# Kernel optimization log

Hardware: AMD Instinct MI355X
Metric: run time of the kernel (lower is better)

## Reference

```python
import jax, jax.numpy as jnp
import numpy as np

P = 512       # protein_dim
D = 512       # drug_dim
N = 2000      # neighbors per layer
E = 300000    # binding edges per layer
ND = 100000   # total drugs
BASELINE = 6.0
LN_EPS = 1e-5


def setup_inputs() -> dict:
    key = jax.random.key(0)
    ks = jax.random.split(key, 24)
    inp = {
        "target_features": jax.random.normal(ks[0], (P,), jnp.float32),
        "form_features": jax.random.normal(ks[1], (N, P), jnp.float32),
        "role_features": jax.random.normal(ks[2], (N, P), jnp.float32),
        "form_neighbors": jnp.arange(N, dtype=jnp.int64) if jax.config.jax_enable_x64 else jnp.arange(N, dtype=jnp.int32),
        "role_neighbors": jnp.arange(N, dtype=jnp.int32),
        "form_binds_ei": jax.random.randint(ks[3], (2, E), 0, N, jnp.int32),
        "form_binds_y": jax.random.uniform(ks[4], (E,), jnp.float32) * 8.0 + 2.0,
        "role_binds_ei": jax.random.randint(ks[5], (2, E), 0, N, jnp.int32),
        "role_binds_y": jax.random.uniform(ks[6], (E,), jnp.float32) * 8.0 + 2.0,
        "drug_features": jax.random.normal(ks[7], (ND, D), jnp.float32),
    }
    inp["form_neighbors"] = jnp.arange(N, dtype=jnp.int32)
    attn_in = P * 2 + 16
    s1 = 1.0 / np.sqrt(attn_in)
    s2 = 1.0 / np.sqrt(64)
    sd = 1.0 / np.sqrt(D)
    sp = 1.0 / np.sqrt(P)
    inp["layer_emb"] = jax.random.normal(ks[8], (2, 16), jnp.float32)
    inp["W1"] = jax.random.uniform(ks[9], (attn_in, 64), jnp.float32, -s1, s1)
    inp["b1"] = jax.random.uniform(ks[10], (64,), jnp.float32, -s1, s1)
    inp["W2"] = jax.random.uniform(ks[11], (64, 1), jnp.float32, -s2, s2)
    inp["b2"] = jax.random.uniform(ks[12], (1,), jnp.float32, -s2, s2)
    inp["Wi1"] = jax.random.uniform(ks[13], (D, P), jnp.float32, -sd, sd)
    inp["bi1"] = jax.random.uniform(ks[14], (P,), jnp.float32, -sd, sd)
    inp["prelu_alpha"] = jnp.array(0.25, jnp.float32)
    inp["Wi2"] = jax.random.uniform(ks[15], (P, P), jnp.float32, -sp, sp)
    inp["bi2"] = jax.random.uniform(ks[16], (P,), jnp.float32, -sp, sp)
    inp["ln_gamma"] = jnp.ones((P,), jnp.float32)
    inp["ln_beta"] = jnp.zeros((P,), jnp.float32)
    return inp


def _pref_vectors(neighbor_ids, ei, y, drug_features):
    # Vectorized form of the per-neighbor masked gather-sum:
    # for each edge, find its neighbor slot (neighbor_ids is sorted);
    # edges whose src id is not a neighbor get zero weight.
    n = neighbor_ids.shape[0]
    pos = jnp.clip(jnp.searchsorted(neighbor_ids, ei[0]), 0, n - 1)
    valid = neighbor_ids[pos] == ei[0]
    w = jnp.where(valid, y - BASELINE, 0.0)              # [E]
    contrib = drug_features[ei[1]] * w[:, None]          # [E, D] gather (memory-bound)
    return jax.ops.segment_sum(contrib, pos, num_segments=n)  # [N, D]


def _attention(z_target, z_neighbors, l_vec, W1, b1, W2, b2):
    n = z_neighbors.shape[0]
    inp = jnp.concatenate(
        [jnp.broadcast_to(z_target, (n, z_target.shape[0])),
         z_neighbors,
         jnp.broadcast_to(l_vec, (n, l_vec.shape[0]))], axis=-1)  # [N, 2P+16]
    h = inp @ W1 + b1
    h = jnp.where(h > 0, h, 0.2 * h)  # LeakyReLU(0.2)
    return h @ W2 + b2                # [N, 1]


def reference(target_features, form_features, role_features, form_neighbors,
              role_neighbors, form_binds_ei, form_binds_y, role_binds_ei,
              role_binds_y, drug_features, layer_emb, W1, b1, W2, b2,
              Wi1, bi1, prelu_alpha, Wi2, bi2, ln_gamma, ln_beta):
    form_msgs = _pref_vectors(form_neighbors, form_binds_ei, form_binds_y, drug_features)
    role_msgs = _pref_vectors(role_neighbors, role_binds_ei, role_binds_y, drug_features)

    form_attn = _attention(target_features, form_features, layer_emb[0], W1, b1, W2, b2)
    role_attn = _attention(target_features, role_features, layer_emb[1], W1, b1, W2, b2)

    all_msgs = jnp.concatenate([form_msgs, role_msgs], axis=0)   # [2N, D]
    all_attn = jnp.concatenate([form_attn, role_attn], axis=0)   # [2N, 1]
    attn_weights = jax.nn.softmax(all_attn, axis=0)
    v_prior = jnp.sum(attn_weights * all_msgs, axis=0)           # [D]

    h = v_prior @ Wi1 + bi1
    h = jnp.where(h > 0, h, prelu_alpha * h)  # PReLU
    v = h @ Wi2 + bi2                          # [P]

    x = target_features + v
    mu = jnp.mean(x)
    var = jnp.mean(jnp.square(x - mu))
    z_refined = (x - mu) / jnp.sqrt(var + LN_EPS) * ln_gamma + ln_beta
    return (z_refined, form_msgs, role_msgs)
```

## Files before the change

### kernel.cpp

```cpp
#include <hip/hip_runtime.h>
#include <math.h>

static constexpr int PD = 512;
static constexpr float BASEV = 6.0f;
static constexpr int CAP = 320;

typedef float f4v __attribute__((ext_vector_type(4)));
typedef int   i4v __attribute__((ext_vector_type(4)));
typedef int   i2v __attribute__((ext_vector_type(2)));

__global__ __launch_bounds__(256) void front_kernel(
    const int* __restrict__ ei_f, const float* __restrict__ y_f,
    const int* __restrict__ ei_r, const float* __restrict__ y_r,
    const int* __restrict__ nb_f, const int* __restrict__ nb_r,
    const float* __restrict__ target, const float* __restrict__ formF,
    const float* __restrict__ roleF, const float* __restrict__ lemb,
    const float* __restrict__ W1, const float* __restrict__ b1,
    const float* __restrict__ W2, const float* __restrict__ b2,
    int N, int E, int AB, int EBf,
    int* __restrict__ cnt, int2* __restrict__ bins,
    float* __restrict__ logits) {
    __shared__ float sred[384];
    int b = blockIdx.x;
    if (b >= AB) {
        int b2 = b - AB;
        bool role = b2 >= EBf;
        const int* nb = role ? nb_r : nb_f;
        const int* ei = role ? ei_r : ei_f;
        const float* yy = role ? y_r : y_f;
        int base = (role ? b2 - EBf : b2) * 1024;
        int nb0 = nb[0];
#pragma unroll
        for (int r = 0; r < 4; r++) {
            int e = base + threadIdx.x + r * 256;
            if (e >= E) continue;
            int v = ei[e];
            int g = v - nb0; g = g < 0 ? 0 : (g >= N ? N - 1 : g);
            int pos;
            if (nb[g] == v && (g == 0 || nb[g - 1] < v)) {
                pos = g;
            } else {
                int lo = 0, hi = N;
                while (lo < hi) { int mid = (lo + hi) >> 1; if (nb[mid] < v) lo = mid + 1; else hi = mid; }
                pos = lo < N ? lo : N - 1;
                if (nb[pos] != v) continue;
            }
            int s = role ? N + pos : pos;
            float w = yy[e] - BASEV;
            int slot = atomicAdd(&cnt[s], 1);
            if (slot < CAP) {
                i2v val; val.x = ei[E + e]; val.y = __float_as_int(w);
                __builtin_nontemporal_store(val, reinterpret_cast<i2v*>(bins + (size_t)s * CAP + slot));
            }
        }
    } else {
        float* spart = sred;
        float* sc0 = spart + 256;
        float* sc1 = spart + 320;
        int jj = threadIdx.x & 63, ck = threadIdx.x >> 6;
        const float* Wc = W1 + jj;
        float tp = 0.f;
        int p0 = ck * 128;
        for (int p = p0; p < p0 + 128; p += 4) {
            float4 tv = *(const float4*)(target + p);
            tp += tv.x * Wc[(size_t)(p + 0) * 64] + tv.y * Wc[(size_t)(p + 1) * 64]
                + tv.z * Wc[(size_t)(p + 2) * 64] + tv.w * Wc[(size_t)(p + 3) * 64];
        }
        spart[ck * 64 + jj] = tp;
        __syncthreads();
        if (ck == 0) {
            float c = b1[jj] + spart[jj] + spart[64 + jj] + spart[128 + jj] + spart[192 + jj];
            float c0 = c, c1 = c;
            for (int q = 0; q < 16; q++) {
                float wq = Wc[(size_t)(2 * PD + q) * 64];
                c0 += lemb[q] * wq;
                c1 += lemb[16 + q] * wq;
            }
            sc0[jj] = c0; sc1[jj] = c1;
        }
        __syncthreads();
        int wave = threadIdx.x >> 6, lane = threadIdx.x & 63;
        int rr = b * 4 + wave;
        int nseg = 2 * N;
        if (rr >= nseg) return;
        bool rl = rr >= N;
        const float* z = rl ? roleF + (size_t)(rr - N) * PD : formF + (size_t)rr * PD;
        const float* Wz = W1 + (size_t)PD * 64 + lane;
        float hA = rl ? sc1[lane] : sc0[lane];
        float hB = 0.f, hC = 0.f, hD = 0.f;
        for (int p = 0; p < PD; p += 8) {
            float4 z0 = *(const float4*)(z + p);
            float4 z1 = *(const float4*)(z + p + 4);
            hA += z0.x * Wz[(size_t)(p + 0) * 64] + z0.y * Wz[(size_t)(p + 1) * 64];
            hB += z0.z * Wz[(size_t)(p + 2) * 64] + z0.w * Wz[(size_t)(p + 3) * 64];
            hC += z1.x * Wz[(size_t)(p + 4) * 64] + z1.y * Wz[(size_t)(p + 5) * 64];
            hD += z1.z * Wz[(size_t)(p + 6) * 64] + z1.w * Wz[(size_t)(p + 7) * 64];
        }
        float hh = (hA + hB) + (hC + hD);
        hh = hh > 0.f ? hh : 0.2f * hh;
        float vv = hh * W2[lane];
#pragma unroll
        for (int off = 32; off > 0; off >>= 1) vv += __shfl_down(vv, off, 64);
        if (lane == 0) logits[rr] = vv + b2[0];
    }
}

__global__ __launch_bounds__(128) void accum_kernel(const int* __restrict__ cnt,
                                                    const int2* __restrict__ bins,
                                                    const float* __restrict__ drug,
                                                    const float* __restrict__ logits,
                                                    int nseg,
                                                    float* __restrict__ sm,
                                                    float* __restrict__ msgs) {
    int b = blockIdx.x;
    int t = threadIdx.x;
    if (b == nseg) {
        __shared__ float red[128];
        float m = -1e30f;
        for (int s = t; s < nseg; s += 128) m = fmaxf(m, logits[s]);
        red[t] = m; __syncthreads();
        for (int o = 64; o > 0; o >>= 1) { if (t < o) red[t] = fmaxf(red[t], red[t + o]); __syncthreads(); }
        m = red[0]; __syncthreads();
        float sum = 0.f;
        for (int s = t; s < nseg; s += 128) sum += expf(logits[s] - m);
        red[t] = sum; __syncthreads();
        for (int o = 64; o > 0; o >>= 1) { if (t < o) red[t] += red[t + o]; __syncthreads(); }
        if (t == 0) { sm[0] = m; sm[1] = red[0]; }
        return;
    }
    int n = cnt[b]; n = n < CAP ? n : CAP;
    const int2* bb = bins + (size_t)b * CAP;
    float4 acc = make_float4(0.f, 0.f, 0.f, 0.f);
    int k = 0;
    for (; k + 15 < n; k += 16) {
        i4v q0 = __builtin_nontemporal_load(reinterpret_cast<const i4v*>(bb + k + 0));
        i4v q1 = __builtin_nontemporal_load(reinterpret_cast<const i4v*>(bb + k + 2));
        i4v q2 = __builtin_nontemporal_load(reinterpret_cast<const i4v*>(bb + k + 4));
        i4v q3 = __builtin_nontemporal_load(reinterpret_cast<const i4v*>(bb + k + 6));
        i4v q4 = __builtin_nontemporal_load(reinterpret_cast<const i4v*>(bb + k + 8));
        i4v q5 = __builtin_nontemporal_load(reinterpret_cast<const i4v*>(bb + k + 10));
        i4v q6 = __builtin_nontemporal_load(reinterpret_cast<const i4v*>(bb + k + 12));
        i4v q7 = __builtin_nontemporal_load(reinterpret_cast<const i4v*>(bb + k + 14));
        float4 d0 = ((const float4*)(drug + (size_t)q0.x * PD))[t];
        float4 d1 = ((const float4*)(drug + (size_t)q0.z * PD))[t];
        float4 d2 = ((const float4*)(drug + (size_t)q1.x * PD))[t];
        float4 d3 = ((const float4*)(drug + (size_t)q1.z * PD))[t];
        float4 d4 = ((const float4*)(drug + (size_t)q2.x * PD))[t];
        float4 d5 = ((const float4*)(drug + (size_t)q2.z * PD))[t];
        float4 d6 = ((const float4*)(drug + (size_t)q3.x * PD))[t];
        float4 d7 = ((const float4*)(drug + (size_t)q3.z * PD))[t];
        float4 d8 = ((const float4*)(drug + (size_t)q4.x * PD))[t];
        float4 d9 = ((const float4*)(drug + (size_t)q4.z * PD))[t];
        float4 da = ((const float4*)(drug + (size_t)q5.x * PD))[t];
        float4 db = ((const float4*)(drug + (size_t)q5.z * PD))[t];
        float4 dc = ((const float4*)(drug + (size_t)q6.x * PD))[t];
        float4 dd = ((const float4*)(drug + (size_t)q6.z * PD))[t];
        float4 de = ((const float4*)(drug + (size_t)q7.x * PD))[t];
        float4 df = ((const float4*)(drug + (size_t)q7.z * PD))[t];
        float w0 = __int_as_float(q0.y), w1 = __int_as_float(q0.w);
        float w2 = __int_as_float(q1.y), w3 = __int_as_float(q1.w);
        float w4 = __int_as_float(q2.y), w5 = __int_as_float(q2.w);
        float w6 = __int_as_float(q3.y), w7 = __int_as_float(q3.w);
        float w8 = __int_as_float(q4.y), w9 = __int_as_float(q4.w);
        float wa = __int_as_float(q5.y), wb = __int_as_float(q5.w);
        float wc = __int_as_float(q6.y), wd = __int_as_float(q6.w);
        float we = __int_as_float(q7.y), wf = __int_as_float(q7.w);
        acc.x += w0 * d0.x; acc.y += w0 * d0.y; acc.z += w0 * d0.z; acc.w += w0 * d0.w;
        acc.x += w1 * d1.x; acc.y += w1 * d1.y; acc.z += w1 * d1.z; acc.w += w1 * d1.w;
        acc.x += w2 * d2.x; acc.y += w2 * d2.y; acc.z += w2 * d2.z; acc.w += w2 * d2.w;
        acc.x += w3 * d3.x; acc.y += w3 * d3.y; acc.z += w3 * d3.z; acc.w += w3 * d3.w;
        acc.x += w4 * d4.x; acc.y += w4 * d4.y; acc.z += w4 * d4.z; acc.w += w4 * d4.w;
        acc.x += w5 * d5.x; acc.y += w5 * d5.y; acc.z += w5 * d5.z; acc.w += w5 * d5.w;
        acc.x += w6 * d6.x; acc.y += w6 * d6.y; acc.z += w6 * d6.z; acc.w += w6 * d6.w;
        acc.x += w7 * d7.x; acc.y += w7 * d7.y; acc.z += w7 * d7.z; acc.w += w7 * d7.w;
        acc.x += w8 * d8.x; acc.y += w8 * d8.y; acc.z += w8 * d8.z; acc.w += w8 * d8.w;
        acc.x += w9 * d9.x; acc.y += w9 * d9.y; acc.z += w9 * d9.z; acc.w += w9 * d9.w;
        acc.x += wa * da.x; acc.y += wa * da.y; acc.z += wa * da.z; acc.w += wa * da.w;
        acc.x += wb * db.x; acc.y += wb * db.y; acc.z += wb * db.z; acc.w += wb * db.w;
        acc.x += wc * dc.x; acc.y += wc * dc.y; acc.z += wc * dc.z; acc.w += wc * dc.w;
        acc.x += wd * dd.x; acc.y += wd * dd.y; acc.z += wd * dd.z; acc.w += wd * dd.w;
        acc.x += we * de.x; acc.y += we * de.y; acc.z += we * de.z; acc.w += we * de.w;
        acc.x += wf * df.x; acc.y += wf * df.y; acc.z += wf * df.z; acc.w += wf * df.w;
    }
    for (; k + 3 < n; k += 4) {
        i4v q0 = __builtin_nontemporal_load(reinterpret_cast<const i4v*>(bb + k + 0));
        i4v q1 = __builtin_nontemporal_load(reinterpret_cast<const i4v*>(bb + k + 2));
        float4 d0 = ((const float4*)(drug + (size_t)q0.x * PD))[t];
        float4 d1 = ((const float4*)(drug + (size_t)q0.z * PD))[t];
        float4 d2 = ((const float4*)(drug + (size_t)q1.x * PD))[t];
        float4 d3 = ((const float4*)(drug + (size_t)q1.z * PD))[t];
        float w0 = __int_as_float(q0.y), w1 = __int_as_float(q0.w);
        float w2 = __int_as_float(q1.y), w3 = __int_as_float(q1.w);
        acc.x += w0 * d0.x; acc.y += w0 * d0.y; acc.z += w0 * d0.z; acc.w += w0 * d0.w;
        acc.x += w1 * d1.x; acc.y += w1 * d1.y; acc.z += w1 * d1.z; acc.w += w1 * d1.w;
        acc.x += w2 * d2.x; acc.y += w2 * d2.y; acc.z += w2 * d2.z; acc.w += w2 * d2.w;
        acc.x += w3 * d3.x; acc.y += w3 * d3.y; acc.z += w3 * d3.z; acc.w += w3 * d3.w;
    }
    for (; k < n; k++) {
        int2 e0 = bb[k];
        float w0 = __int_as_float(e0.y);
        float4 d0 = ((const float4*)(drug + (size_t)e0.x * PD))[t];
        acc.x += w0 * d0.x; acc.y += w0 * d0.y; acc.z += w0 * d0.z; acc.w += w0 * d0.w;
    }
    f4v av; av.x = acc.x; av.y = acc.y; av.z = acc.z; av.w = acc.w;
    __builtin_nontemporal_store(av, reinterpret_cast<f4v*>(msgs + (size_t)b * PD) + t);
}

__global__ __launch_bounds__(128) void vprior_kernel(const float* __restrict__ logits,
                                                     const float* __restrict__ msgs,
                                                     const float* __restrict__ sm,
                                                     int nseg, float* __restrict__ v_prior) {
    int t = threadIdx.x;
    float m = sm[0];
    float inv = 1.f / sm[1];
    float4 acc = make_float4(0.f, 0.f, 0.f, 0.f);
    for (int s = blockIdx.x; s < nseg; s += gridDim.x) {
        float w = expf(logits[s] - m) * inv;
        float4 d = ((const float4*)(msgs + (size_t)s * PD))[t];
        acc.x += w * d.x; acc.y += w * d.y; acc.z += w * d.z; acc.w += w * d.w;
    }
    atomicAdd(&v_prior[4 * t + 0], acc.x);
    atomicAdd(&v_prior[4 * t + 1], acc.y);
    atomicAdd(&v_prior[4 * t + 2], acc.z);
    atomicAdd(&v_prior[4 * t + 3], acc.w);
}

__global__ __launch_bounds__(256) void mv1_kernel(const float* __restrict__ v_prior,
                                                  const float* __restrict__ Wi1,
                                                  float* __restrict__ h) {
    int b = blockIdx.x;
    int t = threadIdx.x;
    float2 acc = make_float2(0.f, 0.f);
    int d0 = b * 16;
    for (int d = d0; d < d0 + 16; d++) {
        float vd = v_prior[d];
        float2 w = ((const float2*)(Wi1 + (size_t)d * PD))[t];
        acc.x += vd * w.x; acc.y += vd * w.y;
    }
    atomicAdd(&h[2 * t + 0], acc.x);
    atomicAdd(&h[2 * t + 1], acc.y);
}

__global__ __launch_bounds__(256) void mv2_kernel(const float* __restrict__ h,
                                                  const float* __restrict__ bi1,
                                                  const float* __restrict__ alpha_p,
                                                  const float* __restrict__ Wi2,
                                                  float* __restrict__ v) {
    int b = blockIdx.x;
    int t = threadIdx.x;
    float alpha = alpha_p[0];
    float2 acc = make_float2(0.f, 0.f);
    int q0 = b * 16;
    for (int q = q0; q < q0 + 16; q++) {
        float hq = h[q] + bi1[q];
        hq = hq > 0.f ? hq : alpha * hq;
        float2 w = ((const float2*)(Wi2 + (size_t)q * PD))[t];
        acc.x += hq * w.x; acc.y += hq * w.y;
    }
    atomicAdd(&v[2 * t + 0], acc.x);
    atomicAdd(&v[2 * t + 1], acc.y);
}

__global__ __launch_bounds__(512) void final_kernel(const float* __restrict__ target,
                                                    const float* __restrict__ v,
                                                    const float* __restrict__ bi2,
                                                    const float* __restrict__ gamma,
                                                    const float* __restrict__ beta,
                                                    float* __restrict__ out) {
    __shared__ float red[512];
    int t = threadIdx.x;
    float x = target[t] + v[t] + bi2[t];
    red[t] = x; __syncthreads();
    for (int o = 256; o > 0; o >>= 1) { if (t < o) red[t] += red[t + o]; __syncthreads(); }
    float mu = red[0] * (1.f / 512.f);
    __syncthreads();
    float dx = x - mu;
    red[t] = dx * dx; __syncthreads();
    for (int o = 256; o > 0; o >>= 1) { if (t < o) red[t] += red[t + o]; __syncthreads(); }
    float var = red[0] * (1.f / 512.f);
    out[t] = dx * (1.f / sqrtf(var + 1e-5f)) * gamma[t] + beta[t];
}

extern "C" void kernel_launch(void* const* d_in, const int* in_sizes, int n_in,
                              void* d_out, int out_size, void* d_ws, size_t ws_size,
                              hipStream_t stream) {
    const float* target = (const float*)d_in[0];
    const float* formF  = (const float*)d_in[1];
    const float* roleF  = (const float*)d_in[2];
    const int*   nb_f   = (const int*)d_in[3];
    const int*   nb_r   = (const int*)d_in[4];
    const int*   ei_f   = (const int*)d_in[5];
    const float* y_f    = (const float*)d_in[6];
    const int*   ei_r   = (const int*)d_in[7];
    const float* y_r    = (const float*)d_in[8];
    const float* drug   = (const float*)d_in[9];
    const float* lemb   = (const float*)d_in[10];
    const float* W1     = (const float*)d_in[11];
    const float* b1     = (const float*)d_in[12];
    const float* W2     = (const float*)d_in[13];
    const float* b2     = (const float*)d_in[14];
    const float* Wi1    = (const float*)d_in[15];
    const float* bi1    = (const float*)d_in[16];
    const float* alpha  = (const float*)d_in[17];
    const float* Wi2    = (const float*)d_in[18];
    const float* bi2    = (const float*)d_in[19];
    const float* gamma  = (const float*)d_in[20];
    const float* beta   = (const float*)d_in[21];

    int N = in_sizes[3];
    int E = in_sizes[5] / 2;
    int nseg = 2 * N;

    int* ws = (int*)d_ws;
    int*   cnt     = ws + 0;
    float* v_prior = (float*)(ws + 4096);
    float* hbuf    = (float*)(ws + 4608);
    float* vbuf    = (float*)(ws + 5120);
    float* logits  = (float*)(ws + 5632);
    float* smbuf   = (float*)(ws + 9728);
    int2*  bins    = (int2*)(ws + 9736);

    float* out  = (float*)d_out;
    float* msgs = out + PD;

    hipMemsetAsync(ws, 0, 5632 * sizeof(int), stream);

    int AB  = (nseg + 3) / 4;
    int EBf = (E + 1023) / 1024;
    front_kernel<<<AB + 2 * EBf, 256, 0, stream>>>(ei_f, y_f, ei_r, y_r, nb_f, nb_r,
                                                   target, formF, roleF, lemb,
                                                   W1, b1, W2, b2, N, E, AB, EBf,
                                                   cnt, bins, logits);
    accum_kernel<<<nseg + 1, 128, 0, stream>>>(cnt, bins, drug, logits, nseg, smbuf, msgs);
    vprior_kernel<<<256, 128, 0, stream>>>(logits, msgs, smbuf, nseg, v_prior);
    mv1_kernel<<<32, 256, 0, stream>>>(v_prior, Wi1, hbuf);
    mv2_kernel<<<32, 256, 0, stream>>>(hbuf, bi1, alpha, Wi2, vbuf);
    final_kernel<<<1, 512, 0, stream>>>(target, vbuf, bi2, gamma, beta, out);
}
```

Before: 442.2 us.

## Move attention logits into accumulate kernel and compute softmax stats per vprior block

Splits the front kernel so edge binning runs alone, then co-schedules the attention-logit MLP blocks (now two rows per 128-thread block) with the drug-gather accumulation blocks in one launch. The dedicated softmax-statistics block is removed; each vprior block now recomputes the max and sum over all logits itself. The aim is to shorten the edge-binning critical path and overlap the attention compute with the bandwidth-bound gather. The cost is redundant softmax reductions across 256 blocks and smaller attention blocks that each recompute the target projection.

```diff
diff --git a/kernel.cpp b/kernel.cpp
--- a/kernel.cpp
+++ b/kernel.cpp
@@ -9,59 +9,66 @@
 typedef int   i4v __attribute__((ext_vector_type(4)));
 typedef int   i2v __attribute__((ext_vector_type(2)));
 
-__global__ __launch_bounds__(256) void front_kernel(
+__global__ __launch_bounds__(256) void edge_kernel(
     const int* __restrict__ ei_f, const float* __restrict__ y_f,
     const int* __restrict__ ei_r, const float* __restrict__ y_r,
     const int* __restrict__ nb_f, const int* __restrict__ nb_r,
+    int N, int E, int EBf,
+    int* __restrict__ cnt, int2* __restrict__ bins) {
+    int b = blockIdx.x;
+    bool role = b >= EBf;
+    const int* nb = role ? nb_r : nb_f;
+    const int* ei = role ? ei_r : ei_f;
+    const float* yy = role ? y_r : y_f;
+    int base = (role ? b - EBf : b) * 1024;
+    int nb0 = nb[0];
+#pragma unroll
+    for (int r = 0; r < 4; r++) {
+        int e = base + threadIdx.x + r * 256;
+        if (e >= E) continue;
+        int v = ei[e];
+        int g = v - nb0; g = g < 0 ? 0 : (g >= N ? N - 1 : g);
+        int pos;
+        if (nb[g] == v && (g == 0 || nb[g - 1] < v)) {
+            pos = g;
+        } else {
+            int lo = 0, hi = N;
+            while (lo < hi) { int mid = (lo + hi) >> 1; if (nb[mid] < v) lo = mid + 1; else hi = mid; }
+            pos = lo < N ? lo : N - 1;
+            if (nb[pos] != v) continue;
+        }
+        int s = role ? N + pos : pos;
+        float w = yy[e] - BASEV;
+        int slot = atomicAdd(&cnt[s], 1);
+        if (slot < CAP) {
+            i2v val; val.x = ei[E + e]; val.y = __float_as_int(w);
+            __builtin_nontemporal_store(val, reinterpret_cast<i2v*>(bins + (size_t)s * CAP + slot));
+        }
+    }
+}
+
+__global__ __launch_bounds__(128) void accum_attn_kernel(
+    const int* __restrict__ cnt, const int2* __restrict__ bins,
+    const float* __restrict__ drug,
     const float* __restrict__ target, const float* __restrict__ formF,
     const float* __restrict__ roleF, const float* __restrict__ lemb,
     const float* __restrict__ W1, const float* __restrict__ b1,
     const float* __restrict__ W2, const float* __restrict__ b2,
-    int N, int E, int AB, int EBf,
-    int* __restrict__ cnt, int2* __restrict__ bins,
-    float* __restrict__ logits) {
-    __shared__ float sred[384];
+    int nseg, float* __restrict__ logits, float* __restrict__ msgs) {
+    __shared__ float sred[256];
     int b = blockIdx.x;
-    if (b >= AB) {
-        int b2 = b - AB;
-        bool role = b2 >= EBf;
-        const int* nb = role ? nb_r : nb_f;
-        const int* ei = role ? ei_r : ei_f;
-        const float* yy = role ? y_r : y_f;
-        int base = (role ? b2 - EBf : b2) * 1024;
-        int nb0 = nb[0];
-#pragma unroll
-        for (int r = 0; r < 4; r++) {
-            int e = base + threadIdx.x + r * 256;
-            if (e >= E) continue;
-            int v = ei[e];
-            int g = v - nb0; g = g < 0 ? 0 : (g >= N ? N - 1 : g);
-            int pos;
-            if (nb[g] == v && (g == 0 || nb[g - 1] < v)) {
-                pos = g;
-            } else {
-                int lo = 0, hi = N;
-                while (lo < hi) { int mid = (lo + hi) >> 1; if (nb[mid] < v) lo = mid + 1; else hi = mid; }
-                pos = lo < N ? lo : N - 1;
-                if (nb[pos] != v) continue;
-            }
-            int s = role ? N + pos : pos;
-            float w = yy[e] - BASEV;
-            int slot = atomicAdd(&cnt[s], 1);
-            if (slot < CAP) {
-                i2v val; val.x = ei[E + e]; val.y = __float_as_int(w);
-                __builtin_nontemporal_store(val, reinterpret_cast<i2v*>(bins + (size_t)s * CAP + slot));
-            }
-        }
-    } else {
+    int t = threadIdx.x;
+    if (b >= nseg) {
+        int N = nseg >> 1;
+        int a = b - nseg;
         float* spart = sred;
-        float* sc0 = spart + 256;
-        float* sc1 = spart + 320;
-        int jj = threadIdx.x & 63, ck = threadIdx.x >> 6;
+        float* sc0 = sred + 128;
+        float* sc1 = sred + 192;
+        int jj = t & 63, ck = t >> 6;
         const float* Wc = W1 + jj;
         float tp = 0.f;
-        int p0 = ck * 128;
-        for (int p = p0; p < p0 + 128; p += 4) {
+        int p0 = ck * 256;
+        for (int p = p0; p < p0 + 256; p += 4) {
             float4 tv = *(const float4*)(target + p);
             tp += tv.x * Wc[(size_t)(p + 0) * 64] + tv.y * Wc[(size_t)(p + 1) * 64]
                 + tv.z * Wc[(size_t)(p + 2) * 64] + tv.w * Wc[(size_t)(p + 3) * 64];
@@ -69,7 +76,7 @@
         spart[ck * 64 + jj] = tp;
         __syncthreads();
         if (ck == 0) {
-            float c = b1[jj] + spart[jj] + spart[64 + jj] + spart[128 + jj] + spart[192 + jj];
+            float c = b1[jj] + spart[jj] + spart[64 + jj];
             float c0 = c, c1 = c;
             for (int q = 0; q < 16; q++) {
                 float wq = Wc[(size_t)(2 * PD + q) * 64];
@@ -79,9 +86,8 @@
             sc0[jj] = c0; sc1[jj] = c1;
         }
         __syncthreads();
-        int wave = threadIdx.x >> 6, lane = threadIdx.x & 63;
-        int rr = b * 4 + wave;
-        int nseg = 2 * N;
+        int wave = ck, lane = jj;
+        int rr = a * 2 + wave;
         if (rr >= nseg) return;
         bool rl = rr >= N;
         const float* z = rl ? roleF + (size_t)(rr - N) * PD : formF + (size_t)rr * PD;
@@ -102,30 +108,6 @@
 #pragma unroll
         for (int off = 32; off > 0; off >>= 1) vv += __shfl_down(vv, off, 64);
         if (lane == 0) logits[rr] = vv + b2[0];
-    }
-}
-
-__global__ __launch_bounds__(128) void accum_kernel(const int* __restrict__ cnt,
-                                                    const int2* __restrict__ bins,
-                                                    const float* __restrict__ drug,
-                                                    const float* __restrict__ logits,
-                                                    int nseg,
-                                                    float* __restrict__ sm,
-                                                    float* __restrict__ msgs) {
-    int b = blockIdx.x;
-    int t = threadIdx.x;
-    if (b == nseg) {
-        __shared__ float red[128];
-        float m = -1e30f;
-        for (int s = t; s < nseg; s += 128) m = fmaxf(m, logits[s]);
-        red[t] = m; __syncthreads();
-        for (int o = 64; o > 0; o >>= 1) { if (t < o) red[t] = fmaxf(red[t], red[t + o]); __syncthreads(); }
-        m = red[0]; __syncthreads();
-        float sum = 0.f;
-        for (int s = t; s < nseg; s += 128) sum += expf(logits[s] - m);
-        red[t] = sum; __syncthreads();
-        for (int o = 64; o > 0; o >>= 1) { if (t < o) red[t] += red[t + o]; __syncthreads(); }
-        if (t == 0) { sm[0] = m; sm[1] = red[0]; }
         return;
     }
     int n = cnt[b]; n = n < CAP ? n : CAP;
@@ -208,11 +190,20 @@
 
 __global__ __launch_bounds__(128) void vprior_kernel(const float* __restrict__ logits,
                                                      const float* __restrict__ msgs,
-                                                     const float* __restrict__ sm,
                                                      int nseg, float* __restrict__ v_prior) {
-    int t = threadIdx.x;
-    float m = sm[0];
-    float inv = 1.f / sm[1];
+    __shared__ float red[128];
+    int t = threadIdx.x;
+    float m = -1e30f;
+    for (int s = t; s < nseg; s += 128) m = fmaxf(m, logits[s]);
+    red[t] = m; __syncthreads();
+    for (int o = 64; o > 0; o >>= 1) { if (t < o) red[t] = fmaxf(red[t], red[t + o]); __syncthreads(); }
+    m = red[0]; __syncthreads();
+    float sum = 0.f;
+    for (int s = t; s < nseg; s += 128) sum += expf(logits[s] - m);
+    red[t] = sum; __syncthreads();
+    for (int o = 64; o > 0; o >>= 1) { if (t < o) red[t] += red[t + o]; __syncthreads(); }
+    float inv = 1.f / red[0];
+
     float4 acc = make_float4(0.f, 0.f, 0.f, 0.f);
     for (int s = blockIdx.x; s < nseg; s += gridDim.x) {
         float w = expf(logits[s] - m) * inv;
@@ -317,22 +308,22 @@
     float* hbuf    = (float*)(ws + 4608);
     float* vbuf    = (float*)(ws + 5120);
     float* logits  = (float*)(ws + 5632);
-    float* smbuf   = (float*)(ws + 9728);
-    int2*  bins    = (int2*)(ws + 9736);
+    int2*  bins    = (int2*)(ws + 9728);
 
     float* out  = (float*)d_out;
     float* msgs = out + PD;
 
     hipMemsetAsync(ws, 0, 5632 * sizeof(int), stream);
 
-    int AB  = (nseg + 3) / 4;
     int EBf = (E + 1023) / 1024;
-    front_kernel<<<AB + 2 * EBf, 256, 0, stream>>>(ei_f, y_f, ei_r, y_r, nb_f, nb_r,
-                                                   target, formF, roleF, lemb,
-                                                   W1, b1, W2, b2, N, E, AB, EBf,
-                                                   cnt, bins, logits);
-    accum_kernel<<<nseg + 1, 128, 0, stream>>>(cnt, bins, drug, logits, nseg, smbuf, msgs);
-    vprior_kernel<<<256, 128, 0, stream>>>(logits, msgs, smbuf, nseg, v_prior);
+    int AB2 = (nseg + 1) / 2;
+    edge_kernel<<<2 * EBf, 256, 0, stream>>>(ei_f, y_f, ei_r, y_r, nb_f, nb_r,
+                                             N, E, EBf, cnt, bins);
+    accum_attn_kernel<<<nseg + AB2, 128, 0, stream>>>(cnt, bins, drug,
+                                                      target, formF, roleF, lemb,
+                                                      W1, b1, W2, b2,
+                                                      nseg, logits, msgs);
+    vprior_kernel<<<256, 128, 0, stream>>>(logits, msgs, nseg, v_prior);
     mv1_kernel<<<32, 256, 0, stream>>>(v_prior, Wi1, hbuf);
     mv2_kernel<<<32, 256, 0, stream>>>(hbuf, bi1, alpha, Wi2, vbuf);
     final_kernel<<<1, 512, 0, stream>>>(target, vbuf, bi2, gamma, beta, out);
```

Measured after the change: 476.0 us. 7.6% more time.
